# Performance work log

Hardware: AMD Instinct MI355X
Metric: run time of the kernel (lower is better)

The kernel has to match this reference:

```python
import jax, jax.numpy as jnp
import numpy as np

GROUPS = 32
EPS = 1e-5
HEAD_DIM = 64


def group_norm(x, gamma, beta):
    # x: [B, L, C]; normalize over (L, C//G) within each of G channel groups
    B, L, C = x.shape
    g = x.reshape(B, L, GROUPS, C // GROUPS)
    mean = g.mean(axis=(1, 3), keepdims=True)
    var = g.var(axis=(1, 3), keepdims=True)
    g = (g - mean) * jax.lax.rsqrt(var + EPS)
    return g.reshape(B, L, C) * gamma + beta


def setup_inputs() -> dict:
    key = jax.random.key(0)
    ks = jax.random.split(key, 4)
    B, H, W, C = 16, 32, 32, 512
    x = jax.random.normal(ks[0], (B, H, W, C), dtype=jnp.float32)
    timesteps = jax.random.randint(ks[1], (B,), 0, 1000)
    gamma = jnp.ones((C,), jnp.float32)
    beta = jnp.zeros((C,), jnp.float32)
    w_qkv = jax.random.normal(ks[2], (C, 3 * C), dtype=jnp.float32) * (1.0 / np.sqrt(C))
    b_qkv = jnp.zeros((3 * C,), jnp.float32)
    w_out = jax.random.normal(ks[3], (C, C), dtype=jnp.float32) * (1.0 / np.sqrt(C))
    b_out = jnp.zeros((C,), jnp.float32)
    return {"x": x, "timesteps": timesteps, "gamma": gamma, "beta": beta,
            "w_qkv": w_qkv, "b_qkv": b_qkv, "w_out": w_out, "b_out": b_out}


def reference(x, timesteps, gamma, beta, w_qkv, b_qkv, w_out, b_out):
    B, H, W, C = x.shape
    L = H * W
    nh = C // HEAD_DIM
    factor = jnp.asarray(1.0 / np.sqrt(np.sqrt(HEAD_DIM)), x.dtype)  # applied to both q and k

    xf = x.reshape(B, L, C)
    qkv = group_norm(xf, gamma, beta) @ w_qkv + b_qkv        # [B, L, 3C]
    q, k, v = jnp.split(qkv, 3, axis=-1)

    def heads(t):  # [B, L, C] -> [B, nh, L, d]
        return t.reshape(B, L, nh, HEAD_DIM).transpose(0, 2, 1, 3)

    q, k, v = heads(q) * factor, heads(k) * factor, heads(v)
    scores = jnp.einsum('bhqd,bhkd->bhqk', q, k)             # [B, nh, L, L]
    attn = jax.nn.softmax(scores, axis=-1)
    out = jnp.einsum('bhqk,bhkd->bhqd', attn, v)             # [B, nh, L, d]
    out = out.transpose(0, 2, 1, 3).reshape(B, L, C)
    h = out @ w_out + b_out
    return (xf + h).reshape(B, H, W, C)
```

## Files before the change

kernel.cpp:

```cpp
#include <hip/hip_runtime.h>

#define Bn 16
#define Ln 1024
#define Cn 512
#define Mn (Bn*Ln)
#define N3n 1536

typedef unsigned short u16;
typedef __attribute__((ext_vector_type(8))) short short8;
typedef __attribute__((ext_vector_type(4))) float f32x4;

typedef const __attribute__((address_space(1))) void* gas_p;
typedef __attribute__((address_space(3))) void* las_p;

__device__ inline void gl_lds16(const void* g, void* l) {
  __builtin_amdgcn_global_load_lds((gas_p)g, (las_p)l, 16, 0, 0);
}

__device__ inline u16 f2bf(float f) {
  union { float f; unsigned u; } v; v.f = f;
  unsigned r = v.u + 0x7FFFu + ((v.u >> 16) & 1u);
  return (u16)(r >> 16);
}

__device__ inline f32x4 mfma16(short8 a, short8 b, f32x4 c) {
  return __builtin_amdgcn_mfma_f32_16x16x32_bf16(a, b, c, 0, 0, 0);
}

__global__ __launch_bounds__(256) void k_gnstats(const float* __restrict__ x,
                                                 float* __restrict__ stats) {
  int bid = blockIdx.x;
  int b = bid >> 5, g = bid & 31;
  const float* base = x + (size_t)b * (Ln * Cn) + g * 16;
  int tid = threadIdx.x;
  float s1 = 0.f, s2 = 0.f;
  for (int i = 0; i < 16; ++i) {
    int s = i * 256 + tid;
    int l = s >> 2, cq = s & 3;
    float4 v = *(const float4*)(base + (size_t)l * Cn + cq * 4);
    s1 += v.x + v.y + v.z + v.w;
    s2 += v.x * v.x + v.y * v.y + v.z * v.z + v.w * v.w;
  }
  for (int off = 32; off > 0; off >>= 1) {
    s1 += __shfl_down(s1, off);
    s2 += __shfl_down(s2, off);
  }
  __shared__ float rb[8];
  int w = tid >> 6, lane = tid & 63;
  if (lane == 0) { rb[w] = s1; rb[4 + w] = s2; }
  __syncthreads();
  if (tid == 0) {
    float a = rb[0] + rb[1] + rb[2] + rb[3];
    float q = rb[4] + rb[5] + rb[6] + rb[7];
    float mean = a * (1.f / 16384.f);
    float var = q * (1.f / 16384.f) - mean * mean;
    stats[bid * 2] = mean;
    stats[bid * 2 + 1] = rsqrtf(var + 1e-5f);
  }
}

__global__ __launch_bounds__(256) void k_gnapply(const float* __restrict__ x,
                                                 const float* __restrict__ stats,
                                                 const float* __restrict__ gamma,
                                                 const float* __restrict__ beta,
                                                 u16* __restrict__ gn) {
  int idx = blockIdx.x * 256 + threadIdx.x;
  size_t e = (size_t)idx << 2;
  int m = (int)(e >> 9), c = (int)(e & 511);
  int b = m >> 10, g = c >> 4;
  float mean = stats[(b * 32 + g) * 2];
  float rstd = stats[(b * 32 + g) * 2 + 1];
  float4 xv = *(const float4*)(x + e);
  float4 gv = *(const float4*)(gamma + c);
  float4 bv = *(const float4*)(beta + c);
  ushort4 o;
  o.x = f2bf((xv.x - mean) * rstd * gv.x + bv.x);
  o.y = f2bf((xv.y - mean) * rstd * gv.y + bv.y);
  o.z = f2bf((xv.z - mean) * rstd * gv.z + bv.z);
  o.w = f2bf((xv.w - mean) * rstd * gv.w + bv.w);
  *(ushort4*)(gn + e) = o;
}

__global__ __launch_bounds__(256) void k_wtrans(const float* __restrict__ wqkv,
                                                const float* __restrict__ wout,
                                                u16* __restrict__ wqkvT,
                                                u16* __restrict__ woutT) {
  int id = blockIdx.x * 256 + threadIdx.x;
  if (id < Cn * N3n) {
    int k = id & 511, n = id >> 9;
    wqkvT[id] = f2bf(wqkv[(size_t)k * N3n + n]);
  } else {
    int id2 = id - Cn * N3n;
    int k = id2 & 511, n = id2 >> 9;
    woutT[id2] = f2bf(wout[(size_t)k * Cn + n]);
  }
}

__global__ __launch_bounds__(256) void k_qkv(const u16* __restrict__ gn,
                                             const u16* __restrict__ wT,
                                             const float* __restrict__ bias,
                                             u16* __restrict__ qb,
                                             u16* __restrict__ kb,
                                             u16* __restrict__ vT) {
  __shared__ __attribute__((aligned(16))) char smem[66560];
  int bid = blockIdx.x;
  int wg = (bid & 7) * 192 + (bid >> 3);
  int tn = wg % 12, tm = wg / 12;
  int m0 = tm * 128, n0 = tn * 128;
  int tid = threadIdx.x;
  int w = tid >> 6, lane = tid & 63, lr = lane & 15, lg = lane >> 4;
  int wr = w >> 1, wc = w & 1;
  const f32x4 fzero = {0.f, 0.f, 0.f, 0.f};
  f32x4 acc[4][4];
#pragma unroll
  for (int mi = 0; mi < 4; ++mi)
#pragma unroll
    for (int ni = 0; ni < 4; ++ni) acc[mi][ni] = fzero;

#pragma unroll
  for (int i = 0; i < 4; ++i) {
    int s = i * 256 + tid;
    int r = s >> 3, c = s & 7;
    gl_lds16(gn + ((size_t)(m0 + r) * 512 + ((c ^ (r & 7)) << 3)),
             smem + ((s & ~63) << 4));
    gl_lds16(wT + ((size_t)(n0 + r) * 512 + ((c ^ (r & 7)) << 3)),
             smem + 32768 + ((s & ~63) << 4));
  }
  __syncthreads();

  for (int kt = 0; kt < 8; ++kt) {
    int cur = kt & 1;
    char* Asb = smem + cur * 16384;
    char* Bsb = smem + 32768 + cur * 16384;
    if (kt < 7) {
      int nb = cur ^ 1, k0n = (kt + 1) * 64;
#pragma unroll
      for (int i = 0; i < 4; ++i) {
        int s = i * 256 + tid;
        int r = s >> 3, c = s & 7;
        gl_lds16(gn + ((size_t)(m0 + r) * 512 + k0n + ((c ^ (r & 7)) << 3)),
                 smem + nb * 16384 + ((s & ~63) << 4));
        gl_lds16(wT + ((size_t)(n0 + r) * 512 + k0n + ((c ^ (r & 7)) << 3)),
                 smem + 32768 + nb * 16384 + ((s & ~63) << 4));
      }
    }
#pragma unroll
    for (int ks = 0; ks < 2; ++ks) {
      short8 af[4], bf[4];
#pragma unroll
      for (int mi = 0; mi < 4; ++mi) {
        int row = wr * 64 + mi * 16 + lr;
        int ck = ks * 4 + lg;
        af[mi] = *(const short8*)(Asb + row * 128 + ((ck ^ (lr & 7)) << 4));
      }
#pragma unroll
      for (int ni = 0; ni < 4; ++ni) {
        int row = wc * 64 + ni * 16 + lr;
        int ck = ks * 4 + lg;
        bf[ni] = *(const short8*)(Bsb + row * 128 + ((ck ^ (lr & 7)) << 4));
      }
#pragma unroll
      for (int mi = 0; mi < 4; ++mi)
#pragma unroll
        for (int ni = 0; ni < 4; ++ni)
          acc[mi][ni] = mfma16(af[mi], bf[ni], acc[mi][ni]);
    }
    __syncthreads();
  }

  if (tn >= 8) {
    float* T = (float*)smem;
#pragma unroll
    for (int mi = 0; mi < 4; ++mi)
#pragma unroll
      for (int ni = 0; ni < 4; ++ni) {
        int n_l = wc * 64 + ni * 16 + lr;
        float bn = bias[n0 + n_l];
#pragma unroll
        for (int rr = 0; rr < 4; ++rr) {
          int m_l = wr * 64 + mi * 16 + lg * 4 + rr;
          T[n_l * 130 + m_l] = acc[mi][ni][rr] + bn;
        }
      }
    __syncthreads();
    int n_l = tid >> 1, half = tid & 1;
    int nv = n0 - 1024 + n_l;
    int h = nv >> 6, dd = nv & 63;
    int bb = m0 >> 10, li0 = m0 & 1023;
    u16* dst = vT + ((size_t)(bb * 8 + h) * 64 + dd) * 1024 + li0;
    const float* Tr = T + n_l * 130;
#pragma unroll
    for (int j = 0; j < 8; ++j) {
      int mb = half * 8 + 16 * j;
      uint4 o;
      o.x = (unsigned)f2bf(Tr[mb + 0]) | ((unsigned)f2bf(Tr[mb + 1]) << 16);
      o.y = (unsigned)f2bf(Tr[mb + 2]) | ((unsigned)f2bf(Tr[mb + 3]) << 16);
      o.z = (unsigned)f2bf(Tr[mb + 4]) | ((unsigned)f2bf(Tr[mb + 5]) << 16);
      o.w = (unsigned)f2bf(Tr[mb + 6]) | ((unsigned)f2bf(Tr[mb + 7]) << 16);
      *(uint4*)(dst + mb) = o;
    }
  } else {
#pragma unroll
    for (int mi = 0; mi < 4; ++mi) {
#pragma unroll
      for (int ni = 0; ni < 4; ++ni) {
        int n = n0 + wc * 64 + ni * 16 + lr;
        float bn = bias[n];
        int which = n >> 9, nn = n & 511;
        int h = nn >> 6, dd = nn & 63;
#pragma unroll
        for (int rr = 0; rr < 4; ++rr) {
          int m = m0 + wr * 64 + mi * 16 + lg * 4 + rr;
          float v = acc[mi][ni][rr] + bn;
          int bb = m >> 10, li = m & 1023;
          if (which == 0)
            qb[((size_t)(bb * 8 + h) * 1024 + li) * 64 + dd] = f2bf(v);
          else
            kb[((size_t)(bb * 8 + h) * 1024 + li) * 64 + dd] = f2bf(v);
        }
      }
    }
  }
}

__global__ __launch_bounds__(512, 4) void k_attn(const u16* __restrict__ qb,
                                                 const u16* __restrict__ kb,
                                                 const u16* __restrict__ vT,
                                                 u16* __restrict__ ob) {
  __shared__ __attribute__((aligned(16))) u16 Ks[3 * 64 * 64];
  __shared__ __attribute__((aligned(16))) u16 Vs[3 * 64 * 64];
  __shared__ __attribute__((aligned(16))) u16 Ps[8 * 32 * 64];
  int bid = blockIdx.x;
  int xq = bid & 7, kk = bid >> 3;
  int bh = ((kk & 15) << 3) | xq;
  int qt = kk >> 4;
  const u16* qh = qb + (size_t)bh * 65536;
  const u16* kh = kb + (size_t)bh * 65536;
  const u16* vh = vT + (size_t)bh * 65536;
  int tid = threadIdx.x, w = tid >> 6, lane = tid & 63, lr = lane & 15, lg = lane >> 4;
  int q0 = qt * 256 + w * 32;
  const f32x4 fzero = {0.f, 0.f, 0.f, 0.f};
  const float C1 = 0.18033688011112042f;

  short8 qf[2][2];
#pragma unroll
  for (int mi = 0; mi < 2; ++mi)
#pragma unroll
    for (int ks = 0; ks < 2; ++ks)
      qf[mi][ks] = *(const short8*)(qh + (size_t)(q0 + mi * 16 + lr) * 64 +
                                    ks * 32 + lg * 8);
  f32x4 accO[2][4];
  float mst[2], lst[2], nmc[2];
#pragma unroll
  for (int mi = 0; mi < 2; ++mi) {
#pragma unroll
    for (int nd = 0; nd < 4; ++nd) accO[mi][nd] = fzero;
    mst[mi] = -1e30f; lst[mi] = 0.f; nmc[mi] = 0.f;
  }
  char* Pwb = (char*)(Ps + w * 2048);

  int sr = tid >> 3, sc8 = tid & 7;
  size_t koff = (size_t)sr * 64 + ((sc8 ^ (sr & 7)) << 3);
  size_t voff = (size_t)sr * 1024 + ((sc8 ^ (sr & 7)) << 3);
  int ldst = (tid & ~63) << 4;

  gl_lds16(kh + koff, (char*)Ks + ldst);
  gl_lds16(vh + voff, (char*)Vs + ldst);
  gl_lds16(kh + 4096 + koff, (char*)Ks + 8192 + ldst);
  gl_lds16(vh + 64 + voff, (char*)Vs + 8192 + ldst);
  asm volatile("s_waitcnt vmcnt(2)" ::: "memory");
  __builtin_amdgcn_s_barrier();

#pragma unroll 1
  for (int jt = 0; jt < 16; ++jt) {
    int cb = jt % 3;
    char* Ksb = (char*)Ks + cb * 8192;
    char* Vsb = (char*)Vs + cb * 8192;
    if (jt < 14) {
      int nb = (jt + 2) % 3;
      gl_lds16(kh + (size_t)(jt + 2) * 4096 + koff, (char*)Ks + nb * 8192 + ldst);
      gl_lds16(vh + (size_t)(jt + 2) * 64 + voff, (char*)Vs + nb * 8192 + ldst);
    }

    short8 kf[4][2];
#pragma unroll
    for (int nj = 0; nj < 4; ++nj)
#pragma unroll
      for (int ks = 0; ks < 2; ++ks) {
        int row = nj * 16 + lr;
        kf[nj][ks] = *(const short8*)(Ksb + row * 128 + (((ks * 4 + lg) ^ (row & 7)) << 4));
      }

    f32x4 sc[2][4];
#pragma unroll
    for (int mi = 0; mi < 2; ++mi)
#pragma unroll
      for (int nj = 0; nj < 4; ++nj) sc[mi][nj] = fzero;
#pragma unroll
    for (int ks = 0; ks < 2; ++ks)
#pragma unroll
      for (int mi = 0; mi < 2; ++mi)
#pragma unroll
        for (int nj = 0; nj < 4; ++nj)
          sc[mi][nj] = mfma16(kf[nj][ks], qf[mi][ks], sc[mi][nj]);

#pragma unroll
    for (int mi = 0; mi < 2; ++mi) {
      float t0 = fmaxf(fmaxf(sc[mi][0][0], sc[mi][0][1]), fmaxf(sc[mi][0][2], sc[mi][0][3]));
      float t1 = fmaxf(fmaxf(sc[mi][1][0], sc[mi][1][1]), fmaxf(sc[mi][1][2], sc[mi][1][3]));
      float t2 = fmaxf(fmaxf(sc[mi][2][0], sc[mi][2][1]), fmaxf(sc[mi][2][2], sc[mi][2][3]));
      float t3 = fmaxf(fmaxf(sc[mi][3][0], sc[mi][3][1]), fmaxf(sc[mi][3][2], sc[mi][3][3]));
      float mloc = fmaxf(fmaxf(t0, t1), fmaxf(t2, t3));
      mloc = fmaxf(mloc, __shfl_xor(mloc, 16));
      mloc = fmaxf(mloc, __shfl_xor(mloc, 32));
      if (__any(mloc - mst[mi] > 8.f)) {
        float mn = fmaxf(mst[mi], mloc);
        float al = __builtin_amdgcn_exp2f((mst[mi] - mn) * C1);
        mst[mi] = mn;
        nmc[mi] = -mn * C1;
        lst[mi] *= al;
#pragma unroll
        for (int rr = 0; rr < 4; ++rr) {
          float ab = __shfl(al, (lane & 48) | ((lane >> 4) & 3) * 4 + rr);
#pragma unroll
          for (int nd = 0; nd < 4; ++nd) accO[mi][nd][rr] *= ab;
        }
      }
      float nm = nmc[mi];
      float rs = 0.f;
#pragma unroll
      for (int nj = 0; nj < 4; ++nj) {
        float p0 = __builtin_amdgcn_exp2f(__builtin_fmaf(sc[mi][nj][0], C1, nm));
        float p1 = __builtin_amdgcn_exp2f(__builtin_fmaf(sc[mi][nj][1], C1, nm));
        float p2 = __builtin_amdgcn_exp2f(__builtin_fmaf(sc[mi][nj][2], C1, nm));
        float p3 = __builtin_amdgcn_exp2f(__builtin_fmaf(sc[mi][nj][3], C1, nm));
        rs += (p0 + p1) + (p2 + p3);
        unsigned u0 = __float_as_uint(p0), u1 = __float_as_uint(p1);
        unsigned u2 = __float_as_uint(p2), u3 = __float_as_uint(p3);
        uint2 pv;
        pv.x = (u0 >> 16) | (u1 & 0xFFFF0000u);
        pv.y = (u2 >> 16) | (u3 & 0xFFFF0000u);
        int row = mi * 16 + lr;
        int byte = row * 128 + (nj * 16 + lg * 4) * 2;
        byte ^= (row & 7) << 4;
        *(uint2*)(Pwb + byte) = pv;
      }
      rs += __shfl_xor(rs, 16);
      rs += __shfl_xor(rs, 32);
      lst[mi] += rs;
    }

    short8 bv[4][2];
#pragma unroll
    for (int nd = 0; nd < 4; ++nd)
#pragma unroll
      for (int ks = 0; ks < 2; ++ks) {
        int row = nd * 16 + lr;
        bv[nd][ks] = *(const short8*)(Vsb + row * 128 + (((ks * 4 + lg) ^ (row & 7)) << 4));
      }

    short8 ap[2][2];
#pragma unroll
    for (int mi = 0; mi < 2; ++mi)
#pragma unroll
      for (int ks = 0; ks < 2; ++ks) {
        int row = mi * 16 + lr;
        int byte = row * 128 + (ks * 32 + lg * 8) * 2;
        byte ^= (row & 7) << 4;
        ap[mi][ks] = *(const short8*)(Pwb + byte);
      }
#pragma unroll
    for (int ks = 0; ks < 2; ++ks)
#pragma unroll
      for (int mi = 0; mi < 2; ++mi)
#pragma unroll
        for (int nd = 0; nd < 4; ++nd)
          accO[mi][nd] = mfma16(ap[mi][ks], bv[nd][ks], accO[mi][nd]);

    if (jt < 14)
      asm volatile("s_waitcnt vmcnt(2)" ::: "memory");
    else
      asm volatile("s_waitcnt vmcnt(0)" ::: "memory");
    __builtin_amdgcn_s_barrier();
  }

  int b = bh >> 3, h = bh & 7;
#pragma unroll
  for (int mi = 0; mi < 2; ++mi) {
    float il = 1.f / lst[mi];
#pragma unroll
    for (int rr = 0; rr < 4; ++rr) {
      float ib = __shfl(il, (lane & 48) | ((lane >> 4) & 3) * 4 + rr);
      int row = q0 + mi * 16 + lg * 4 + rr;
#pragma unroll
      for (int nd = 0; nd < 4; ++nd) {
        int col = h * 64 + nd * 16 + lr;
        ob[(size_t)(b * 1024 + row) * 512 + col] = f2bf(accO[mi][nd][rr] * ib);
      }
    }
  }
}

__global__ __launch_bounds__(256) void k_out(const u16* __restrict__ ob,
                                             const u16* __restrict__ wT,
                                             const float* __restrict__ bias,
                                             const float* __restrict__ x,
                                             float* __restrict__ out) {
  __shared__ __attribute__((aligned(16))) u16 As[2 * 128 * 64];
  __shared__ __attribute__((aligned(16))) u16 Bs[2 * 128 * 64];
  int bid = blockIdx.x;
  int wg = (bid & 7) * 64 + (bid >> 3);
  int tn = wg & 3, tm = wg >> 2;
  int m0 = tm * 128, n0 = tn * 128;
  int tid = threadIdx.x;
  int w = tid >> 6, lane = tid & 63, lr = lane & 15, lg = lane >> 4;
  int wr = w >> 1, wc = w & 1;
  const f32x4 fzero = {0.f, 0.f, 0.f, 0.f};
  f32x4 acc[4][4];
#pragma unroll
  for (int mi = 0; mi < 4; ++mi)
#pragma unroll
    for (int ni = 0; ni < 4; ++ni) acc[mi][ni] = fzero;

#pragma unroll
  for (int i = 0; i < 4; ++i) {
    int s = i * 256 + tid;
    int r = s >> 3, c = s & 7;
    gl_lds16(ob + ((size_t)(m0 + r) * 512 + ((c ^ (r & 7)) << 3)),
             (char*)As + ((s & ~63) << 4));
    gl_lds16(wT + ((size_t)(n0 + r) * 512 + ((c ^ (r & 7)) << 3)),
             (char*)Bs + ((s & ~63) << 4));
  }
  __syncthreads();

  for (int kt = 0; kt < 8; ++kt) {
    int cur = kt & 1;
    char* Asb = (char*)As + cur * 16384;
    char* Bsb = (char*)Bs + cur * 16384;
    if (kt < 7) {
      int nb = cur ^ 1, k0n = (kt + 1) * 64;
#pragma unroll
      for (int i = 0; i < 4; ++i) {
        int s = i * 256 + tid;
        int r = s >> 3, c = s & 7;
        gl_lds16(ob + ((size_t)(m0 + r) * 512 + k0n + ((c ^ (r & 7)) << 3)),
                 (char*)As + nb * 16384 + ((s & ~63) << 4));
        gl_lds16(wT + ((size_t)(n0 + r) * 512 + k0n + ((c ^ (r & 7)) << 3)),
                 (char*)Bs + nb * 16384 + ((s & ~63) << 4));
      }
    }
#pragma unroll
    for (int ks = 0; ks < 2; ++ks) {
      short8 af[4], bf[4];
#pragma unroll
      for (int mi = 0; mi < 4; ++mi) {
        int row = wr * 64 + mi * 16 + lr;
        int ck = ks * 4 + lg;
        af[mi] = *(const short8*)(Asb + row * 128 + ((ck ^ (lr & 7)) << 4));
      }
#pragma unroll
      for (int ni = 0; ni < 4; ++ni) {
        int row = wc * 64 + ni * 16 + lr;
        int ck = ks * 4 + lg;
        bf[ni] = *(const short8*)(Bsb + row * 128 + ((ck ^ (lr & 7)) << 4));
      }
#pragma unroll
      for (int mi = 0; mi < 4; ++mi)
#pragma unroll
        for (int ni = 0; ni < 4; ++ni)
          acc[mi][ni] = mfma16(af[mi], bf[ni], acc[mi][ni]);
    }
    __syncthreads();
  }
#pragma unroll
  for (int mi = 0; mi < 4; ++mi) {
#pragma unroll
    for (int ni = 0; ni < 4; ++ni) {
      int n = n0 + wc * 64 + ni * 16 + lr;
      float bn = bias[n];
#pragma unroll
      for (int rr = 0; rr < 4; ++rr) {
        int m = m0 + wr * 64 + mi * 16 + lg * 4 + rr;
        size_t off = (size_t)m * 512 + n;
        out[off] = x[off] + acc[mi][ni][rr] + bn;
      }
    }
  }
}

extern "C" void kernel_launch(void* const* d_in, const int* in_sizes, int n_in,
                              void* d_out, int out_size, void* d_ws, size_t ws_size,
                              hipStream_t stream) {
  const float* x = (const float*)d_in[0];
  const float* gamma = (const float*)d_in[2];
  const float* beta = (const float*)d_in[3];
  const float* wqkv = (const float*)d_in[4];
  const float* bqkv = (const float*)d_in[5];
  const float* wout = (const float*)d_in[6];
  const float* bout = (const float*)d_in[7];
  float* out = (float*)d_out;

  char* ws = (char*)d_ws;
  float* stats = (float*)ws;
  u16* gn = (u16*)(ws + 4096);
  u16* wqkvT = (u16*)(ws + 4096 + 16777216);
  u16* woutT = (u16*)(ws + 4096 + 16777216 + 1572864);
  u16* qb = (u16*)(ws + 4096 + 16777216 + 1572864 + 524288);
  u16* kb = qb + 8388608;
  u16* vT = kb + 8388608;
  u16* ob = vT + 8388608;

  k_gnstats<<<512, 256, 0, stream>>>(x, stats);
  k_gnapply<<<8192, 256, 0, stream>>>(x, stats, gamma, beta, gn);
  k_wtrans<<<4096, 256, 0, stream>>>(wqkv, wout, wqkvT, woutT);
  k_qkv<<<1536, 256, 0, stream>>>(gn, wqkvT, bqkv, qb, kb, vT);
  k_attn<<<512, 512, 0, stream>>>(qb, kb, vT, ob);
  k_out<<<512, 256, 0, stream>>>(ob, woutT, bout, x, out);
}
```

Before: 144.2 us.

## Fuse group-norm stats and apply into one kernel staging x in LDS

Merges the two group-norm kernels into one. Each block loads a 1024x32 slice (two groups) of x into 128KB of shared memory, reduces the statistics, then normalizes from LDS and writes bf16. This avoids reading x a second time from global memory and drops one launch, at the cost of very low occupancy (256 blocks, large LDS footprint). Separately, the attention kernel defers the cross-lane row-sum shuffles from every tile iteration to the final normalization, removing per-iteration shuffles.

```diff
diff --git a/kernel.cpp b/kernel.cpp
--- a/kernel.cpp
+++ b/kernel.cpp
@@ -27,58 +27,60 @@
   return __builtin_amdgcn_mfma_f32_16x16x32_bf16(a, b, c, 0, 0, 0);
 }
 
-__global__ __launch_bounds__(256) void k_gnstats(const float* __restrict__ x,
-                                                 float* __restrict__ stats) {
+__global__ __launch_bounds__(256) void k_gn(const float* __restrict__ x,
+                                            const float* __restrict__ gamma,
+                                            const float* __restrict__ beta,
+                                            u16* __restrict__ gn) {
+  __shared__ __attribute__((aligned(16))) float xs[1024 * 32];
+  __shared__ float red[32];
+  __shared__ float stat[4];
   int bid = blockIdx.x;
-  int b = bid >> 5, g = bid & 31;
-  const float* base = x + (size_t)b * (Ln * Cn) + g * 16;
+  int b = bid >> 4, gp = bid & 15;
+  const float* base = x + (size_t)b * (Ln * Cn) + gp * 32;
   int tid = threadIdx.x;
+  int c = tid & 7;
   float s1 = 0.f, s2 = 0.f;
-  for (int i = 0; i < 16; ++i) {
+  for (int i = 0; i < 32; ++i) {
     int s = i * 256 + tid;
-    int l = s >> 2, cq = s & 3;
-    float4 v = *(const float4*)(base + (size_t)l * Cn + cq * 4);
+    int r = s >> 3;
+    float4 v = *(const float4*)(base + (size_t)r * Cn + c * 4);
+    *(float4*)(xs + (size_t)s * 4) = v;
     s1 += v.x + v.y + v.z + v.w;
     s2 += v.x * v.x + v.y * v.y + v.z * v.z + v.w * v.w;
   }
-  for (int off = 32; off > 0; off >>= 1) {
-    s1 += __shfl_down(s1, off);
-    s2 += __shfl_down(s2, off);
-  }
-  __shared__ float rb[8];
+  s1 += __shfl_xor(s1, 1);  s2 += __shfl_xor(s2, 1);
+  s1 += __shfl_xor(s1, 2);  s2 += __shfl_xor(s2, 2);
+  s1 += __shfl_xor(s1, 8);  s2 += __shfl_xor(s2, 8);
+  s1 += __shfl_xor(s1, 16); s2 += __shfl_xor(s2, 16);
+  s1 += __shfl_xor(s1, 32); s2 += __shfl_xor(s2, 32);
   int w = tid >> 6, lane = tid & 63;
-  if (lane == 0) { rb[w] = s1; rb[4 + w] = s2; }
+  if (lane == 0) { red[w * 2 + 0] = s1; red[16 + w * 2 + 0] = s2; }
+  if (lane == 4) { red[w * 2 + 1] = s1; red[16 + w * 2 + 1] = s2; }
   __syncthreads();
-  if (tid == 0) {
-    float a = rb[0] + rb[1] + rb[2] + rb[3];
-    float q = rb[4] + rb[5] + rb[6] + rb[7];
+  if (tid < 2) {
+    float a = red[tid] + red[2 + tid] + red[4 + tid] + red[6 + tid];
+    float q = red[16 + tid] + red[18 + tid] + red[20 + tid] + red[22 + tid];
     float mean = a * (1.f / 16384.f);
     float var = q * (1.f / 16384.f) - mean * mean;
-    stats[bid * 2] = mean;
-    stats[bid * 2 + 1] = rsqrtf(var + 1e-5f);
-  }
-}
-
-__global__ __launch_bounds__(256) void k_gnapply(const float* __restrict__ x,
-                                                 const float* __restrict__ stats,
-                                                 const float* __restrict__ gamma,
-                                                 const float* __restrict__ beta,
-                                                 u16* __restrict__ gn) {
-  int idx = blockIdx.x * 256 + threadIdx.x;
-  size_t e = (size_t)idx << 2;
-  int m = (int)(e >> 9), c = (int)(e & 511);
-  int b = m >> 10, g = c >> 4;
-  float mean = stats[(b * 32 + g) * 2];
-  float rstd = stats[(b * 32 + g) * 2 + 1];
-  float4 xv = *(const float4*)(x + e);
-  float4 gv = *(const float4*)(gamma + c);
-  float4 bv = *(const float4*)(beta + c);
-  ushort4 o;
-  o.x = f2bf((xv.x - mean) * rstd * gv.x + bv.x);
-  o.y = f2bf((xv.y - mean) * rstd * gv.y + bv.y);
-  o.z = f2bf((xv.z - mean) * rstd * gv.z + bv.z);
-  o.w = f2bf((xv.w - mean) * rstd * gv.w + bv.w);
-  *(ushort4*)(gn + e) = o;
+    stat[tid * 2] = mean;
+    stat[tid * 2 + 1] = rsqrtf(var + 1e-5f);
+  }
+  __syncthreads();
+  float mean = stat[(c >> 2) * 2], rstd = stat[(c >> 2) * 2 + 1];
+  float4 gv = *(const float4*)(gamma + gp * 32 + c * 4);
+  float4 bv = *(const float4*)(beta + gp * 32 + c * 4);
+  u16* gdst = gn + (size_t)b * (Ln * Cn) + gp * 32;
+  for (int i = 0; i < 32; ++i) {
+    int s = i * 256 + tid;
+    int r = s >> 3;
+    float4 v = *(const float4*)(xs + (size_t)s * 4);
+    ushort4 o;
+    o.x = f2bf((v.x - mean) * rstd * gv.x + bv.x);
+    o.y = f2bf((v.y - mean) * rstd * gv.y + bv.y);
+    o.z = f2bf((v.z - mean) * rstd * gv.z + bv.z);
+    o.w = f2bf((v.w - mean) * rstd * gv.w + bv.w);
+    *(ushort4*)(gdst + (size_t)r * Cn + c * 4) = o;
+  }
 }
 
 __global__ __launch_bounds__(256) void k_wtrans(const float* __restrict__ wqkv,
@@ -345,8 +347,6 @@
         byte ^= (row & 7) << 4;
         *(uint2*)(Pwb + byte) = pv;
       }
-      rs += __shfl_xor(rs, 16);
-      rs += __shfl_xor(rs, 32);
       lst[mi] += rs;
     }
 
@@ -387,7 +387,10 @@
   int b = bh >> 3, h = bh & 7;
 #pragma unroll
   for (int mi = 0; mi < 2; ++mi) {
-    float il = 1.f / lst[mi];
+    float lt = lst[mi];
+    lt += __shfl_xor(lt, 16);
+    lt += __shfl_xor(lt, 32);
+    float il = 1.f / lt;
 #pragma unroll
     for (int rr = 0; rr < 4; ++rr) {
       float ib = __shfl(il, (lane & 48) | ((lane >> 4) & 3) * 4 + rr);
@@ -501,7 +504,6 @@
   float* out = (float*)d_out;
 
   char* ws = (char*)d_ws;
-  float* stats = (float*)ws;
   u16* gn = (u16*)(ws + 4096);
   u16* wqkvT = (u16*)(ws + 4096 + 16777216);
   u16* woutT = (u16*)(ws + 4096 + 16777216 + 1572864);
@@ -510,8 +512,7 @@
   u16* vT = kb + 8388608;
   u16* ob = vT + 8388608;
 
-  k_gnstats<<<512, 256, 0, stream>>>(x, stats);
-  k_gnapply<<<8192, 256, 0, stream>>>(x, stats, gamma, beta, gn);
+  k_gn<<<256, 256, 0, stream>>>(x, gamma, beta, gn);
   k_wtrans<<<4096, 256, 0, stream>>>(wqkv, wout, wqkvT, woutT);
   k_qkv<<<1536, 256, 0, stream>>>(gn, wqkvT, bqkv, qb, kb, vT);
   k_attn<<<512, 512, 0, stream>>>(qb, kb, vT, ob);
```

After: 139.8 us. -3.0%, faster.
